# Kernel optimization log

Measured on AMD Instinct MI355X. Metric: run time of the kernel, lower is better.

Reference implementation:

```python
import jax, jax.numpy as jnp
import numpy as np

CHUNK = 128  # time_chunk_size from init_kwargs
EPS = 1e-8


def _forward(v, k, alpha, q):
    # v: (T,B,d), k/alpha/q: (T,B,n)
    T, B, d = v.shape
    n = k.shape[-1]
    nc = T // CHUNK  # T assumed divisible by CHUNK
    vr = v.reshape(nc, CHUNK, B, d)
    kr = k.reshape(nc, CHUNK, B, n)
    ar = alpha.reshape(nc, CHUNK, B, n)
    qr = q.reshape(nc, CHUNK, B, n)

    def step(S_prev, xs):
        vc, kc, ac, qc = xs  # (C,B,d), (C,B,n), ...
        outer = jnp.einsum('tbd,tbn->tbdn', vc, kc)          # (C,B,d,n)
        log_a = jnp.log(jnp.clip(ac, EPS))
        log_cp = jnp.cumsum(log_a, axis=0)                   # (C,B,n)
        cp = jnp.exp(log_cp)
        decay = cp / (cp[-1:] + EPS)                         # normalized per chunk
        S_local = jnp.cumsum(outer * decay[:, :, None, :], axis=0)
        prefix = jnp.exp(log_cp[0])                          # (B,n) decay of first step
        S_local = S_local + (S_prev * prefix[:, None, :])[None]
        y = jnp.einsum('tbdn,tbn->tbd', S_local, qc)         # (C,B,d)
        return S_local[-1], y

    S0 = jnp.zeros((B, d, n), v.dtype)
    _, ys = jax.lax.scan(step, S0, (vr, kr, ar, qr))
    return ys.reshape(T, B, d)


def setup_inputs() -> dict:
    key = jax.random.key(0)
    k1, k2, k3, k4 = jax.random.split(key, 4)
    T, B, d, n = 2048, 4, 256, 256
    return {
        'v': jax.random.normal(k1, (T, B, d), jnp.float32),
        'k': jax.random.normal(k2, (T, B, n), jnp.float32),
        'alpha': jax.random.uniform(k3, (T, B, n), jnp.float32),
        'q': jax.random.normal(k4, (T, B, n), jnp.float32),
    }


def reference(v, k, alpha, q):
    return _forward(v, k, alpha, q)
```

## Files before the change

kernel.cpp:

```cpp
#include <hip/hip_runtime.h>
#include <math.h>

typedef unsigned short u16;
typedef unsigned int u32;
typedef __bf16 bf16x8 __attribute__((ext_vector_type(8)));
typedef float f32x4 __attribute__((ext_vector_type(4)));

#define BB   4
#define DD   256
#define NN   256
#define CH   128
#define NCH  16
#define EPSF 1e-8f

#define WS_QB  0u
#define WS_VT  (4u<<20)
#define WS_WT  (8u<<20)
#define WS_WN  (12u<<20)
#define WS_AST (16u<<20)
#define WS_SPT (18u<<20)
#define WS_PF  (26u<<20)
#define WS_UT  (28u<<20)

__device__ __forceinline__ u16 f2bf(float x) {
  u32 u = __float_as_uint(x);
  u32 r = (u + 0x7fffu + ((u >> 16) & 1u)) >> 16;
  return (u16)r;
}
__device__ __forceinline__ float bf2f(u32 lo16) {
  return __uint_as_float(lo16 << 16);
}

__device__ __forceinline__ int xcd_swz(int bid, int nwg) {
  return (bid & 7) * (nwg >> 3) + (bid >> 3);
}

__device__ __forceinline__ void gload16(void* lds, const void* g) {
  __builtin_amdgcn_global_load_lds((const __attribute__((address_space(1))) void*)g,
                                   (__attribute__((address_space(3))) void*)lds, 16, 0, 0);
}

__device__ __forceinline__ void stage_tile(u16* lds, const u16* g, int rowstride) {
  int tid = threadIdx.x;
#pragma unroll
  for (int h = 0; h < 2; h++) {
    int ci = tid + h * 256;
    int r = ci >> 3, sl = ci & 7;
    const u16* src = g + (size_t)r * rowstride + ((sl ^ (r & 7)) << 3);
    gload16(lds + (size_t)ci * 8, src);
  }
}

__device__ __forceinline__ void read_frags(const u16* buf, int rbase, int lane,
                                           bf16x8 (&f)[2][2]) {
#pragma unroll
  for (int i = 0; i < 2; i++)
#pragma unroll
    for (int ks = 0; ks < 2; ks++) {
      int r = rbase + i * 16 + (lane & 15);
      int slot = ((ks << 2) + (lane >> 4)) ^ (r & 7);
      f[i][ks] = *reinterpret_cast<const bf16x8*>(buf + r * 64 + slot * 8);
    }
}

__device__ __forceinline__ void mma_step(const u16* Ab, const u16* Bb, int rm, int cn,
                                         int lane, f32x4 (&acc)[2][2]) {
  bf16x8 a[2][2], b[2][2];
  read_frags(Ab, rm, lane, a);
  read_frags(Bb, cn, lane, b);
#pragma unroll
  for (int mf = 0; mf < 2; mf++)
#pragma unroll
    for (int nf = 0; nf < 2; nf++)
#pragma unroll
      for (int ks = 0; ks < 2; ks++)
        acc[mf][nf] = __builtin_amdgcn_mfma_f32_16x16x32_bf16(a[mf][ks], b[nf][ks],
                                                              acc[mf][nf], 0, 0, 0);
}

__global__ __launch_bounds__(256) void k_prep(const float* __restrict__ q,
                                              const float* __restrict__ v,
                                              const float* __restrict__ kin,
                                              const float* __restrict__ alpha,
                                              u16* __restrict__ qb,
                                              u16* __restrict__ vT,
                                              u16* __restrict__ wT,
                                              u16* __restrict__ wn,
                                              float* __restrict__ pf) {
  __shared__ __align__(16) char smem[64 * 136 * 2];
  int bid = blockIdx.x;
  int tid = threadIdx.x;
  if (bid < 256) {
    int ng = bid & 3, b = (bid >> 2) & 3, c = bid >> 4;
    int lane16 = tid & 15, seg = tid >> 4;
    int n0 = ng * 64 + lane16 * 4;
    int cb = c * BB + b;
    size_t gbase = ((size_t)(c * CH + seg * 8) * 1024) + b * NN + n0;

    float4 lg[8], kv[8];
    float4 a0 = {0.f, 0.f, 0.f, 0.f};
    float4 run = {0.f, 0.f, 0.f, 0.f};
#pragma unroll
    for (int i = 0; i < 8; i++) {
      float4 av = *(const float4*)&alpha[gbase + (size_t)i * 1024];
      av.x = fmaxf(av.x, EPSF); av.y = fmaxf(av.y, EPSF);
      av.z = fmaxf(av.z, EPSF); av.w = fmaxf(av.w, EPSF);
      kv[i] = *(const float4*)&kin[gbase + (size_t)i * 1024];
      if (i == 0) a0 = av;
      run.x += __logf(av.x); run.y += __logf(av.y);
      run.z += __logf(av.z); run.w += __logf(av.w);
      lg[i] = run;
    }

    float4 (*tot)[16] = (float4(*)[16])smem;
    tot[seg][lane16] = run;
    __syncthreads();
    float4 prefix = {0.f, 0.f, 0.f, 0.f}, total = {0.f, 0.f, 0.f, 0.f};
#pragma unroll
    for (int j = 0; j < 16; j++) {
      float4 tv = tot[j][lane16];
      if (j < seg) { prefix.x += tv.x; prefix.y += tv.y; prefix.z += tv.z; prefix.w += tv.w; }
      total.x += tv.x; total.y += tv.y; total.z += tv.z; total.w += tv.w;
    }
    float4 rden;
    rden.x = 1.f / (__expf(total.x) + EPSF);
    rden.y = 1.f / (__expf(total.y) + EPSF);
    rden.z = 1.f / (__expf(total.z) + EPSF);
    rden.w = 1.f / (__expf(total.w) + EPSF);

    union { u16 u[8]; uint4 v4; } pkn[4];
    u16* wncb = wn + (size_t)cb * (CH * NN);
#pragma unroll
    for (int i = 0; i < 8; i++) {
      union { u16 u[4]; uint2 v2; } row;
      row.u[0] = f2bf(kv[i].x * (__expf(prefix.x + lg[i].x) * rden.x));
      row.u[1] = f2bf(kv[i].y * (__expf(prefix.y + lg[i].y) * rden.y));
      row.u[2] = f2bf(kv[i].z * (__expf(prefix.z + lg[i].z) * rden.z));
      row.u[3] = f2bf(kv[i].w * (__expf(prefix.w + lg[i].w) * rden.w));
      pkn[0].u[i] = row.u[0]; pkn[1].u[i] = row.u[1];
      pkn[2].u[i] = row.u[2]; pkn[3].u[i] = row.u[3];
      *(uint2*)(wncb + (size_t)(seg * 8 + i) * NN + n0) = row.v2;
    }
    u16* wtcb = wT + (size_t)cb * (NN * CH);
#pragma unroll
    for (int j = 0; j < 4; j++)
      *(uint4*)(wtcb + (size_t)(n0 + j) * CH + seg * 8) = pkn[j].v4;
    if (seg == 0) *(float4*)&pf[cb * NN + n0] = a0;
  } else if (bid < 512) {
    int b2 = bid - 256;
    int dt = b2 & 3, cb = b2 >> 2;
    int c = cb >> 2, b = cb & 3;
    int d0 = dt * 64;
    u16* vt = (u16*)smem;
    int sr = tid >> 4, chd = tid & 15;
#pragma unroll
    for (int p = 0; p < 8; p++) {
      int s = p * 16 + sr;
      float4 x = *(const float4*)&v[((size_t)(c * CH + s) * BB + b) * DD + d0 + chd * 4];
      int dbase = chd * 4;
      vt[(dbase + 0) * 136 + s] = f2bf(x.x);
      vt[(dbase + 1) * 136 + s] = f2bf(x.y);
      vt[(dbase + 2) * 136 + s] = f2bf(x.z);
      vt[(dbase + 3) * 136 + s] = f2bf(x.w);
    }
    __syncthreads();
    int dr = tid >> 2, ch = tid & 3;
    const uint4* srcl = (const uint4*)&vt[dr * 136 + ch * 32];
    uint4 a0 = srcl[0], a1 = srcl[1], a2 = srcl[2], a3 = srcl[3];
    uint4* dst = (uint4*)&vT[((size_t)cb * DD + d0 + dr) * CH + ch * 32];
    dst[0] = a0; dst[1] = a1; dst[2] = a2; dst[3] = a3;
  } else {
    size_t gid = (size_t)(bid - 512) * 256 + tid;
    const float4* src = (const float4*)q + gid * 2;
    float4 x = src[0], z = src[1];
    union { u16 u[8]; uint4 v4; } pk;
    pk.u[0] = f2bf(x.x); pk.u[1] = f2bf(x.y); pk.u[2] = f2bf(x.z); pk.u[3] = f2bf(x.w);
    pk.u[4] = f2bf(z.x); pk.u[5] = f2bf(z.y); pk.u[6] = f2bf(z.z); pk.u[7] = f2bf(z.w);
    ((uint4*)qb)[gid] = pk.v4;
  }
}

__global__ __launch_bounds__(256) void k_ut(const u16* __restrict__ vT,
                                            const u16* __restrict__ wT,
                                            u16* __restrict__ utb) {
  __shared__ u16 Al[2][4096], Bl[2][4096];
  int bid = xcd_swz(blockIdx.x, 1024);
  int tid = threadIdx.x, lane = tid & 63, wv = tid >> 6;
  int rm = (wv >> 1) * 32, cn = (wv & 1) * 32;
  int nt = bid & 3, dt = (bid >> 2) & 3, cb = bid >> 4;
  const u16* A = vT + ((size_t)cb * DD + dt * 64) * CH;
  const u16* B = wT + ((size_t)cb * NN + nt * 64) * CH;
  f32x4 acc[2][2] = {};
  stage_tile(Al[0], A, CH); stage_tile(Al[1], A + 64, CH);
  stage_tile(Bl[0], B, CH); stage_tile(Bl[1], B + 64, CH);
  __syncthreads();
  mma_step(Al[0], Bl[0], rm, cn, lane, acc);
  mma_step(Al[1], Bl[1], rm, cn, lane, acc);
  u16* out = utb + ((size_t)cb * DD + dt * 64) * NN + nt * 64;
#pragma unroll
  for (int mf = 0; mf < 2; mf++)
#pragma unroll
    for (int nf = 0; nf < 2; nf++)
#pragma unroll
      for (int r = 0; r < 4; r++) {
        int row = rm + mf * 16 + (lane >> 4) * 4 + r;
        int col = cn + nf * 16 + (lane & 15);
        out[(size_t)row * NN + col] = f2bf(acc[mf][nf][r]);
      }
}

__global__ __launch_bounds__(256) void k_scanas(const u16* __restrict__ qb,
                                                const u16* __restrict__ wn,
                                                const u32* __restrict__ utT2,
                                                const float* __restrict__ pf,
                                                u16* __restrict__ asT,
                                                u32* __restrict__ sptT2) {
  __shared__ u16 Al[2][4096], Bl[2][4096];
  int bid = blockIdx.x;
  int tid = threadIdx.x;
  if (bid < 192) {
    int lane = tid & 63, wv = tid >> 6;
    int rm = (wv >> 1) * 32, cn = (wv & 1) * 32;
    int tile = bid % 3;
    int cb = bid / 3;
    int ti = (tile == 0) ? 0 : 1;
    int si = (tile == 2) ? 1 : 0;
    int t0 = ti * 64, s0 = si * 64;
    int c = cb >> 2, b = cb & 3;
    const u16* A = qb + ((size_t)(c * CH + t0) * BB + b) * NN;
    const u16* B = wn + (size_t)cb * (CH * NN) + (size_t)s0 * NN;
    f32x4 acc[2][2] = {};
    stage_tile(Al[0], A, BB * NN); stage_tile(Bl[0], B, NN);
    __syncthreads();
    for (int st = 0; st < 4; st++) {
      int nx = st + 1;
      if (nx < 4) {
        stage_tile(Al[nx & 1], A + nx * 64, BB * NN);
        stage_tile(Bl[nx & 1], B + nx * 64, NN);
      }
      mma_step(Al[st & 1], Bl[st & 1], rm, cn, lane, acc);
      __syncthreads();
    }
    u16* outb = asT + (size_t)cb * (CH * CH);
#pragma unroll
    for (int mf = 0; mf < 2; mf++)
#pragma unroll
      for (int nf = 0; nf < 2; nf++)
#pragma unroll
        for (int r = 0; r < 4; r++) {
          int t = t0 + rm + mf * 16 + (lane >> 4) * 4 + r;
          int s = s0 + cn + nf * 16 + (lane & 15);
          float val = (s <= t) ? acc[mf][nf][r] : 0.f;
          outb[(size_t)t * CH + s] = f2bf(val);
        }
  } else {
    int id = (bid - 192) * 256 + tid;
    int nh = id & 127, dd = (id >> 7) & 255, b = id >> 15;
    u32 u[NCH];
    float2 pp[NCH];
#pragma unroll
    for (int ch = 0; ch < NCH; ch++) {
      int cb = ch * BB + b;
      u[ch] = utT2[((size_t)cb * DD + dd) * 128 + nh];
      pp[ch] = *(const float2*)&pf[cb * NN + nh * 2];
    }
    float S0 = 0.f, S1 = 0.f;
#pragma unroll
    for (int ch = 0; ch < NCH; ch++) {
      int cb = ch * BB + b;
      float Sp0 = S0 * pp[ch].x, Sp1 = S1 * pp[ch].y;
      sptT2[((size_t)cb * DD + dd) * 128 + nh] = (u32)f2bf(Sp0) | ((u32)f2bf(Sp1) << 16);
      S0 = Sp0 + bf2f(u[ch] & 0xffffu);
      S1 = Sp1 + bf2f(u[ch] >> 16);
    }
  }
}

__global__ __launch_bounds__(256) void k_out(const u16* __restrict__ qb,
                                             const u16* __restrict__ sptT,
                                             const u16* __restrict__ asT,
                                             const u16* __restrict__ vT,
                                             float* __restrict__ y) {
  int bid = xcd_swz(blockIdx.x, 512);
  int dt = bid & 3, tt = (bid >> 2) & 1, cb = bid >> 3;
  int c = cb >> 2, b = cb & 3;
  int t0 = tt * 64, d0 = dt * 64;
  int tid = threadIdx.x, lane = tid & 63, wv = tid >> 6;
  int rm = (wv >> 1) * 32, cn = (wv & 1) * 32;
  const u16* A1 = qb + ((size_t)(c * CH + t0) * BB + b) * NN;
  const u16* B1 = sptT + ((size_t)cb * DD + d0) * NN;
  const u16* A2 = asT + (size_t)cb * (CH * CH) + (size_t)t0 * CH;
  const u16* B2 = vT + ((size_t)cb * DD + d0) * CH;
  __shared__ u16 Al[3][4096], Bl[3][4096];
  f32x4 acc[2][2] = {};
  int nst = 5 + tt;

#define STG_OUT(s)                                                   \
  do {                                                               \
    if ((s) < 4) {                                                   \
      stage_tile(Al[(s) % 3], A1 + (s) * 64, BB * NN);               \
      stage_tile(Bl[(s) % 3], B1 + (s) * 64, NN);                    \
    } else {                                                         \
      stage_tile(Al[(s) % 3], A2 + ((s) - 4) * 64, CH);              \
      stage_tile(Bl[(s) % 3], B2 + ((s) - 4) * 64, CH);              \
    }                                                                \
  } while (0)

  STG_OUT(0);
  STG_OUT(1);
  asm volatile("s_waitcnt vmcnt(4)" ::: "memory");
  __builtin_amdgcn_sched_barrier(0);
  __builtin_amdgcn_s_barrier();

  for (int st = 0; st < nst; st++) {
    bool more = (st + 2 < nst);
    if (more) STG_OUT(st + 2);
    mma_step(Al[st % 3], Bl[st % 3], rm, cn, lane, acc);
    if (st + 1 < nst) {
      if (more) asm volatile("s_waitcnt vmcnt(4)" ::: "memory");
      else      asm volatile("s_waitcnt vmcnt(0)" ::: "memory");
      __builtin_amdgcn_sched_barrier(0);
      __builtin_amdgcn_s_barrier();
    }
  }
#undef STG_OUT

  float* out = y + ((size_t)(c * CH + t0) * BB + b) * DD + d0;
#pragma unroll
  for (int mf = 0; mf < 2; mf++)
#pragma unroll
    for (int nf = 0; nf < 2; nf++)
#pragma unroll
      for (int r = 0; r < 4; r++) {
        int row = rm + mf * 16 + (lane >> 4) * 4 + r;
        int col = cn + nf * 16 + (lane & 15);
        out[(size_t)row * (BB * DD) + col] = acc[mf][nf][r];
      }
}

extern "C" void kernel_launch(void* const* d_in, const int* in_sizes, int n_in,
                              void* d_out, int out_size, void* d_ws, size_t ws_size,
                              hipStream_t stream) {
  const float* v = (const float*)d_in[0];
  const float* k = (const float*)d_in[1];
  const float* alpha = (const float*)d_in[2];
  const float* q = (const float*)d_in[3];
  float* y = (float*)d_out;
  char* ws = (char*)d_ws;
  u16* qb = (u16*)(ws + WS_QB);
  u16* vT = (u16*)(ws + WS_VT);
  u16* wT = (u16*)(ws + WS_WT);
  u16* wn = (u16*)(ws + WS_WN);
  u16* asT = (u16*)(ws + WS_AST);
  u16* sptT = (u16*)(ws + WS_SPT);
  float* pf = (float*)(ws + WS_PF);
  u16* utb = (u16*)(ws + WS_UT);

  k_prep<<<1536, 256, 0, stream>>>(q, v, k, alpha, qb, vT, wT, wn, pf);
  k_ut<<<1024, 256, 0, stream>>>(vT, wT, utb);
  k_scanas<<<704, 256, 0, stream>>>(qb, wn, (const u32*)utb, pf, asT, (u32*)sptT);
  k_out<<<512, 256, 0, stream>>>(qb, sptT, asT, vT, y);
}
```

Baseline: 33.45 us.

## Enlarge k_ut and k_out tiles to 128 rows with 512-thread blocks

k_ut now computes a 128x128 output tile per 512-thread block (four row-fragments per wave) instead of 64x64 per 256-thread block, which cuts redundant loads of the A/B operands. k_out merges the two 64-row time tiles into one 128-row block so the shared spT and vT B-tiles are loaded once, and it skips the upper-triangular attention stage for the first half. The k_out pipeline also drops from triple buffering with explicit vmcnt waits to double buffering with __syncthreads, which may expose more load latency. Block counts halve or quarter, which lowers parallelism across the GPU's compute units.

Result: slower. 34.39 us (+2.8%).

```diff
diff --git a/kernel.cpp b/kernel.cpp
--- a/kernel.cpp
+++ b/kernel.cpp
@@ -51,10 +51,40 @@
   }
 }
 
+__device__ __forceinline__ void stageA512(u16* lds, const u16* g, int rowstride) {
+  int tid = threadIdx.x;
+#pragma unroll
+  for (int h = 0; h < 2; h++) {
+    int ci = tid + h * 512;
+    int r = ci >> 3, sl = ci & 7;
+    const u16* src = g + (size_t)r * rowstride + ((sl ^ (r & 7)) << 3);
+    gload16(lds + (size_t)ci * 8, src);
+  }
+}
+
+__device__ __forceinline__ void stageB512(u16* lds, const u16* g, int rowstride) {
+  int ci = threadIdx.x;
+  int r = ci >> 3, sl = ci & 7;
+  const u16* src = g + (size_t)r * rowstride + ((sl ^ (r & 7)) << 3);
+  gload16(lds + (size_t)ci * 8, src);
+}
+
 __device__ __forceinline__ void read_frags(const u16* buf, int rbase, int lane,
                                            bf16x8 (&f)[2][2]) {
 #pragma unroll
   for (int i = 0; i < 2; i++)
+#pragma unroll
+    for (int ks = 0; ks < 2; ks++) {
+      int r = rbase + i * 16 + (lane & 15);
+      int slot = ((ks << 2) + (lane >> 4)) ^ (r & 7);
+      f[i][ks] = *reinterpret_cast<const bf16x8*>(buf + r * 64 + slot * 8);
+    }
+}
+
+__device__ __forceinline__ void read_frags4(const u16* buf, int rbase, int lane,
+                                            bf16x8 (&f)[4][2]) {
+#pragma unroll
+  for (int i = 0; i < 4; i++)
 #pragma unroll
     for (int ks = 0; ks < 2; ks++) {
       int r = rbase + i * 16 + (lane & 15);
@@ -70,6 +100,21 @@
   read_frags(Bb, cn, lane, b);
 #pragma unroll
   for (int mf = 0; mf < 2; mf++)
+#pragma unroll
+    for (int nf = 0; nf < 2; nf++)
+#pragma unroll
+      for (int ks = 0; ks < 2; ks++)
+        acc[mf][nf] = __builtin_amdgcn_mfma_f32_16x16x32_bf16(a[mf][ks], b[nf][ks],
+                                                              acc[mf][nf], 0, 0, 0);
+}
+
+__device__ __forceinline__ void mma_step8(const u16* Ab, const u16* Bb, int rm, int cn,
+                                          int lane, f32x4 (&acc)[4][2]) {
+  bf16x8 a[4][2], b[2][2];
+  read_frags4(Ab, rm, lane, a);
+  read_frags(Bb, cn, lane, b);
+#pragma unroll
+  for (int mf = 0; mf < 4; mf++)
 #pragma unroll
     for (int nf = 0; nf < 2; nf++)
 #pragma unroll
@@ -180,25 +225,25 @@
   }
 }
 
-__global__ __launch_bounds__(256) void k_ut(const u16* __restrict__ vT,
+__global__ __launch_bounds__(512) void k_ut(const u16* __restrict__ vT,
                                             const u16* __restrict__ wT,
                                             u16* __restrict__ utb) {
-  __shared__ u16 Al[2][4096], Bl[2][4096];
-  int bid = xcd_swz(blockIdx.x, 1024);
+  __shared__ u16 Al[2][8192], Bl[2][8192];
+  int bid = xcd_swz(blockIdx.x, 256);
   int tid = threadIdx.x, lane = tid & 63, wv = tid >> 6;
-  int rm = (wv >> 1) * 32, cn = (wv & 1) * 32;
-  int nt = bid & 3, dt = (bid >> 2) & 3, cb = bid >> 4;
-  const u16* A = vT + ((size_t)cb * DD + dt * 64) * CH;
-  const u16* B = wT + ((size_t)cb * NN + nt * 64) * CH;
-  f32x4 acc[2][2] = {};
-  stage_tile(Al[0], A, CH); stage_tile(Al[1], A + 64, CH);
-  stage_tile(Bl[0], B, CH); stage_tile(Bl[1], B + 64, CH);
+  int rm = (wv >> 2) * 64, cn = (wv & 3) * 32;
+  int nt = bid & 1, dt = (bid >> 1) & 1, cb = bid >> 2;
+  const u16* A = vT + ((size_t)cb * DD + dt * 128) * CH;
+  const u16* B = wT + ((size_t)cb * NN + nt * 128) * CH;
+  f32x4 acc[4][2] = {};
+  stageA512(Al[0], A, CH);      stageA512(Al[1], A + 64, CH);
+  stageA512(Bl[0], B, CH);      stageA512(Bl[1], B + 64, CH);
   __syncthreads();
-  mma_step(Al[0], Bl[0], rm, cn, lane, acc);
-  mma_step(Al[1], Bl[1], rm, cn, lane, acc);
-  u16* out = utb + ((size_t)cb * DD + dt * 64) * NN + nt * 64;
-#pragma unroll
-  for (int mf = 0; mf < 2; mf++)
+  mma_step8(Al[0], Bl[0], rm, cn, lane, acc);
+  mma_step8(Al[1], Bl[1], rm, cn, lane, acc);
+  u16* out = utb + ((size_t)cb * DD + dt * 128) * NN + nt * 128;
+#pragma unroll
+  for (int mf = 0; mf < 4; mf++)
 #pragma unroll
     for (int nf = 0; nf < 2; nf++)
 #pragma unroll
@@ -276,56 +321,46 @@
   }
 }
 
-__global__ __launch_bounds__(256) void k_out(const u16* __restrict__ qb,
+__global__ __launch_bounds__(512) void k_out(const u16* __restrict__ qb,
                                              const u16* __restrict__ sptT,
                                              const u16* __restrict__ asT,
                                              const u16* __restrict__ vT,
                                              float* __restrict__ y) {
-  int bid = xcd_swz(blockIdx.x, 512);
-  int dt = bid & 3, tt = (bid >> 2) & 1, cb = bid >> 3;
+  int bid = xcd_swz(blockIdx.x, 256);
+  int dt = bid & 3, cb = bid >> 2;
   int c = cb >> 2, b = cb & 3;
-  int t0 = tt * 64, d0 = dt * 64;
+  int d0 = dt * 64;
   int tid = threadIdx.x, lane = tid & 63, wv = tid >> 6;
   int rm = (wv >> 1) * 32, cn = (wv & 1) * 32;
-  const u16* A1 = qb + ((size_t)(c * CH + t0) * BB + b) * NN;
+  const u16* A1 = qb + ((size_t)(c * CH) * BB + b) * NN;
   const u16* B1 = sptT + ((size_t)cb * DD + d0) * NN;
-  const u16* A2 = asT + (size_t)cb * (CH * CH) + (size_t)t0 * CH;
+  const u16* A2 = asT + (size_t)cb * (CH * CH);
   const u16* B2 = vT + ((size_t)cb * DD + d0) * CH;
-  __shared__ u16 Al[3][4096], Bl[3][4096];
+  __shared__ u16 Al[2][8192], Bl[2][4096];
   f32x4 acc[2][2] = {};
-  int nst = 5 + tt;
-
-#define STG_OUT(s)                                                   \
+
+#define STG_OUT(s, bi)                                               \
   do {                                                               \
     if ((s) < 4) {                                                   \
-      stage_tile(Al[(s) % 3], A1 + (s) * 64, BB * NN);               \
-      stage_tile(Bl[(s) % 3], B1 + (s) * 64, NN);                    \
+      stageA512(Al[bi], A1 + (s) * 64, BB * NN);                     \
+      stageB512(Bl[bi], B1 + (s) * 64, NN);                          \
     } else {                                                         \
-      stage_tile(Al[(s) % 3], A2 + ((s) - 4) * 64, CH);              \
-      stage_tile(Bl[(s) % 3], B2 + ((s) - 4) * 64, CH);              \
+      stageA512(Al[bi], A2 + ((s) - 4) * 64, CH);                    \
+      stageB512(Bl[bi], B2 + ((s) - 4) * 64, CH);                    \
     }                                                                \
   } while (0)
 
-  STG_OUT(0);
-  STG_OUT(1);
-  asm volatile("s_waitcnt vmcnt(4)" ::: "memory");
-  __builtin_amdgcn_sched_barrier(0);
-  __builtin_amdgcn_s_barrier();
-
-  for (int st = 0; st < nst; st++) {
-    bool more = (st + 2 < nst);
-    if (more) STG_OUT(st + 2);
-    mma_step(Al[st % 3], Bl[st % 3], rm, cn, lane, acc);
-    if (st + 1 < nst) {
-      if (more) asm volatile("s_waitcnt vmcnt(4)" ::: "memory");
-      else      asm volatile("s_waitcnt vmcnt(0)" ::: "memory");
-      __builtin_amdgcn_sched_barrier(0);
-      __builtin_amdgcn_s_barrier();
-    }
+  STG_OUT(0, 0);
+  __syncthreads();
+  for (int st = 0; st < 6; st++) {
+    if (st + 1 < 6) STG_OUT(st + 1, (st + 1) & 1);
+    if (st < 5 || rm >= 64)
+      mma_step(Al[st & 1], Bl[st & 1], rm, cn, lane, acc);
+    __syncthreads();
   }
 #undef STG_OUT
 
-  float* out = y + ((size_t)(c * CH + t0) * BB + b) * DD + d0;
+  float* out = y + ((size_t)(c * CH) * BB + b) * DD + d0;
 #pragma unroll
   for (int mf = 0; mf < 2; mf++)
 #pragma unroll
@@ -357,7 +392,7 @@
   u16* utb = (u16*)(ws + WS_UT);
 
   k_prep<<<1536, 256, 0, stream>>>(q, v, k, alpha, qb, vT, wT, wn, pf);
-  k_ut<<<1024, 256, 0, stream>>>(vT, wT, utb);
+  k_ut<<<256, 512, 0, stream>>>(vT, wT, utb);
   k_scanas<<<704, 256, 0, stream>>>(qb, wn, (const u32*)utb, pf, asT, (u32*)sptT);
-  k_out<<<512, 256, 0, stream>>>(qb, sptT, asT, vT, y);
-}
+  k_out<<<256, 512, 0, stream>>>(qb, sptT, asT, vT, y);
+}
```
